# Kernel tuning notes

Measured on AMD Instinct MI355X. Metric: run time of the kernel, lower is better.

Reference implementation:

```python
import jax, jax.numpy as jnp
import numpy as np

B, C, H, W, CLASSES = 128, 30, 15, 15, 16
ROUTINGS = 3
IN_NUM_CAPS = 32 * 11 * 11  # 3872
IN_DIM, OUT_DIM = 8, 16


def squash(x, axis=-1):
    norm = jnp.linalg.norm(x, axis=axis, keepdims=True)
    scale = norm ** 2 / (1 + norm ** 2) / (norm + 1e-8)
    return scale * x


def conv2d(x, w, b):
    y = jax.lax.conv_general_dilated(x, w, (1, 1), 'VALID',
                                     dimension_numbers=('NCHW', 'OIHW', 'NCHW'))
    return y + b[None, :, None, None]


def setup_inputs() -> dict:
    key = jax.random.key(0)
    ks = jax.random.split(key, 12)
    x = jax.random.normal(ks[0], (B, C, H, W), jnp.float32)
    labels = jax.random.randint(ks[1], (B,), 0, CLASSES)
    y = jax.nn.one_hot(labels, CLASSES, dtype=jnp.float32)
    conv1_w = 0.05 * jax.random.normal(ks[2], (256, C, 3, 3), jnp.float32)
    conv1_b = jnp.zeros((256,), jnp.float32)
    bn_gamma = jnp.ones((256,), jnp.float32)
    bn_beta = jnp.zeros((256,), jnp.float32)
    conv2_w = 0.05 * jax.random.normal(ks[3], (256, 256, 3, 3), jnp.float32)
    conv2_b = jnp.zeros((256,), jnp.float32)
    caps_w = 0.01 * jax.random.normal(ks[4], (CLASSES, IN_NUM_CAPS, OUT_DIM, IN_DIM), jnp.float32)
    dec_w1 = 0.05 * jax.random.normal(ks[5], (OUT_DIM * CLASSES, 328), jnp.float32)
    dec_b1 = jnp.zeros((328,), jnp.float32)
    dec_w2 = 0.05 * jax.random.normal(ks[6], (328, 192), jnp.float32)
    dec_b2 = jnp.zeros((192,), jnp.float32)
    dec_w3 = 0.05 * jax.random.normal(ks[7], (192, C * H * W), jnp.float32)
    dec_b3 = jnp.zeros((C * H * W,), jnp.float32)
    return dict(x=x, y=y, conv1_w=conv1_w, conv1_b=conv1_b, bn_gamma=bn_gamma,
                bn_beta=bn_beta, conv2_w=conv2_w, conv2_b=conv2_b, caps_w=caps_w,
                dec_w1=dec_w1, dec_b1=dec_b1, dec_w2=dec_w2, dec_b2=dec_b2,
                dec_w3=dec_w3, dec_b3=dec_b3)


def reference(x, y, conv1_w, conv1_b, bn_gamma, bn_beta, conv2_w, conv2_b,
              caps_w, dec_w1, dec_b1, dec_w2, dec_b2, dec_w3, dec_b3):
    # conv stem: conv -> batchnorm (batch stats, train mode) -> relu
    h = conv2d(x, conv1_w, conv1_b)                        # [B,256,13,13]
    mean = h.mean(axis=(0, 2, 3), keepdims=True)
    var = h.var(axis=(0, 2, 3), keepdims=True)
    h = (h - mean) / jnp.sqrt(var + 1e-5)
    h = h * bn_gamma[None, :, None, None] + bn_beta[None, :, None, None]
    h = jax.nn.relu(h)

    # primary capsules
    p = conv2d(h, conv2_w, conv2_b)                        # [B,256,11,11]
    caps = squash(p.reshape(B, -1, IN_DIM))                # [B,3872,8]

    # dense capsule: prediction vectors + dynamic routing
    x_hat = jnp.einsum('onij,bnj->boni', caps_w, caps)     # [B,16,3872,16]
    x_hat_det = jax.lax.stop_gradient(x_hat)
    b_log = jnp.zeros(x_hat.shape[:3], x_hat.dtype)        # [B,16,3872]
    out = None
    for i in range(ROUTINGS):
        c = jax.nn.softmax(b_log, axis=1)
        xh = x_hat if i == ROUTINGS - 1 else x_hat_det
        out = squash(jnp.einsum('bon,bond->bod', c, xh))   # [B,16,16]
        if i < ROUTINGS - 1:
            b_log = b_log + jnp.einsum('bod,bond->bon', out, x_hat_det)

    length = jnp.linalg.norm(out, axis=-1)                 # [B,16]

    # decoder MLP on label-masked capsules
    masked = (out * y[:, :, None]).reshape(B, -1)          # [B,256]
    r = jax.nn.sigmoid(masked @ dec_w1 + dec_b1)
    r = jax.nn.sigmoid(r @ dec_w2 + dec_b2)
    recon = (r @ dec_w3 + dec_b3).reshape(B, C, H, W)
    return length, recon
```

## Files before the change

### kernel.cpp

```cpp
#include <hip/hip_runtime.h>
#include <hip/hip_bf16.h>

#define NB 128
#define CIN 30
#define HW 15
#define OC 256
#define H1 13
#define H2 11
#define NCAPS 3872
#define IND 8
#define OUTD 16
#define CLS 16
#define D1 328
#define D2 192
#define OUTPIX 6750
#define NSPLIT 121
#define NPB 32
#define RN 2
#define ROUNDS 16

typedef __attribute__((ext_vector_type(8))) short short8_t;
typedef __attribute__((ext_vector_type(4))) float f32x4;
typedef __attribute__((ext_vector_type(4))) unsigned int u32x4;

__device__ inline unsigned bf16rne(float f) {
  unsigned u = __builtin_bit_cast(unsigned, f);
  return (u + 0x7FFF + ((u >> 16) & 1)) >> 16;
}

#define BLO(u) __builtin_bit_cast(float, (unsigned)((u) << 16))
#define BHI(u) __builtin_bit_cast(float, (unsigned)((u) & 0xffff0000u))

__global__ __launch_bounds__(256) void pack_w1_k(const float* __restrict__ w,
    unsigned short* __restrict__ wpk1) {
  int tid = blockIdx.x * blockDim.x + threadIdx.x;
  int j = tid & 7;
  int oc = (tid >> 3) & 255;
  int kc = (tid >> 11) & 3;
  int tap = tid >> 13;
  int ic = kc * 8 + j;
  float v = (ic < CIN) ? w[((size_t)oc * CIN + ic) * 9 + tap] : 0.f;
  wpk1[tid] = (unsigned short)bf16rne(v);
}

__global__ __launch_bounds__(512, 1) void conv1_mfma_k(
    const float* __restrict__ x, const unsigned short* __restrict__ wpk1,
    const float* __restrict__ bias, float* __restrict__ h,
    float* __restrict__ hsum, float* __restrict__ hsum2) {
  __shared__ char smem[128 * 176 * 4];
  unsigned* hs32 = (unsigned*)smem;
  int bid = blockIdx.x;
  int b = bid >> 1;
  int nh = bid & 1;
  int t = threadIdx.x;
  int l = t & 63;
  int wid = t >> 6;

  if (t < 225) {
    const float* xb = x + (size_t)b * (CIN * 225);
#pragma unroll
    for (int icp = 0; icp < 15; icp++) {
      unsigned u0 = bf16rne(xb[(2 * icp) * 225 + t]);
      unsigned u1 = bf16rne(xb[(2 * icp + 1) * 225 + t]);
      hs32[t * 18 + icp] = u0 | (u1 << 16);
    }
    hs32[t * 18 + 15] = 0;
  }
  __syncthreads();

  int row = l & 15, kc = l >> 4;
  int ocb = nh * 128 + wid * 16;

  int arow[11];
#pragma unroll
  for (int mf = 0; mf < 11; mf++) {
    int m = mf * 16 + row;
    int pix = 0;
    if (m < 169) { int oy = m / 13, ox = m - oy * 13; pix = oy * HW + ox; }
    arow[mf] = pix * 72 + kc * 16;
  }

  f32x4 acc[11];
#pragma unroll
  for (int mf = 0; mf < 11; mf++) acc[mf] = (f32x4){0.f, 0.f, 0.f, 0.f};

  const size_t lanebase = ((size_t)ocb + row) * 8;
  const char* lds_base = (const char*)smem;

#pragma unroll
  for (int tap = 0; tap < 9; tap++) {
    const int ky = tap / 3, kx = tap % 3;
    const int koff = (ky * HW + kx) * 72;
    short8_t bfr = *(const short8_t*)(wpk1 + (size_t)(tap * 4 + kc) * 2048 + lanebase);
#pragma unroll
    for (int mf = 0; mf < 11; mf++) {
      short8_t af = *(const short8_t*)(lds_base + arow[mf] + koff);
      acc[mf] = __builtin_amdgcn_mfma_f32_16x16x32_bf16(af, bfr, acc[mf], 0, 0, 0);
    }
  }

  __syncthreads();
  float* cl = (float*)smem;
  {
    int ocl = wid * 16 + row;
#pragma unroll
    for (int mf = 0; mf < 11; mf++) {
      int m0 = mf * 16 + kc * 4;
      *(f32x4*)&cl[ocl * 176 + m0] = acc[mf];
    }
  }
  __syncthreads();
  for (int idx = t; idx < 128 * 169; idx += 512) {
    int ocl = idx / 169;
    int m = idx - ocl * 169;
    int oc = nh * 128 + ocl;
    h[((size_t)b * 256 + oc) * 169 + m] = cl[ocl * 176 + m] + bias[oc];
  }
  {
    int ocl = t >> 2, sub = t & 3;
    float bs = bias[nh * 128 + ocl];
    float s1 = 0.f, s2 = 0.f;
    int m0 = sub * 43, m1 = m0 + 43; if (m1 > 169) m1 = 169;
    for (int m = m0; m < m1; m++) {
      float v = cl[ocl * 176 + m] + bs;
      s1 += v; s2 += v * v;
    }
    s1 += __shfl_xor(s1, 1); s2 += __shfl_xor(s2, 1);
    s1 += __shfl_xor(s1, 2); s2 += __shfl_xor(s2, 2);
    if (sub == 0) {
      hsum[b * 256 + nh * 128 + ocl] = s1;
      hsum2[b * 256 + nh * 128 + ocl] = s2;
    }
  }
}

__global__ __launch_bounds__(128) void bn_finalize_k(const float* __restrict__ hsum,
    const float* __restrict__ hsum2, float* __restrict__ mean, float* __restrict__ istd) {
  int c = blockIdx.x * 128 + threadIdx.x;
  float s = 0.f, s2 = 0.f;
  for (int b = 0; b < NB; b++) {
    s += hsum[b * 256 + c];
    s2 += hsum2[b * 256 + c];
  }
  const float inv_n = 1.0f / (NB * H1 * H1);
  float m = s * inv_n;
  float v = s2 * inv_n - m * m;
  mean[c] = m;
  istd[c] = rsqrtf(v + 1e-5f);
}

__global__ __launch_bounds__(256) void pack_w2_k(const float* __restrict__ w,
    unsigned short* __restrict__ wpk) {
  int tid = blockIdx.x * blockDim.x + threadIdx.x;
  int e = tid & 7;
  int oc = (tid >> 3) & 255;
  int icchunk = (tid >> 11) & 31;
  int kykx = tid >> 16;
  int ic = icchunk * 8 + e;
  wpk[tid] = (unsigned short)bf16rne(w[((size_t)oc * 256 + ic) * 9 + kykx]);
}

__global__ __launch_bounds__(512, 1) void conv2_mfma_k(
    const float* __restrict__ h, const unsigned short* __restrict__ wpk,
    const float* __restrict__ bias, float* __restrict__ caps,
    const float* __restrict__ mean, const float* __restrict__ istd,
    const float* __restrict__ gamma, const float* __restrict__ beta) {
  __shared__ char smem[169 * 544];
  unsigned* hs32 = (unsigned*)smem;
  int bid = blockIdx.x;
  int b = bid >> 1;
  int nh = bid & 1;
  int t = threadIdx.x;
  int l = t & 63, wid = t >> 6;

  {
    const float* hb = h + (size_t)b * 256 * 169;
    for (int icp = wid; icp < 128; icp += 8) {
      const float* s0 = hb + (size_t)icp * 2 * 169;
      int c0i = icp * 2, c1i = icp * 2 + 1;
      float a0 = istd[c0i] * gamma[c0i], sh0 = beta[c0i] - mean[c0i] * a0;
      float a1 = istd[c1i] * gamma[c1i], sh1 = beta[c1i] - mean[c1i] * a1;
#pragma unroll
      for (int pb = 0; pb < 3; pb++) {
        int pix = pb * 64 + l;
        if (pix < 169) {
          float v0 = fmaxf(fmaf(s0[pix], a0, sh0), 0.f);
          float v1 = fmaxf(fmaf(s0[169 + pix], a1, sh1), 0.f);
          hs32[pix * 136 + icp] = bf16rne(v0) | (bf16rne(v1) << 16);
        }
      }
    }
  }
  __syncthreads();

  int wm = wid & 1;
  int wn = wid >> 1;
  int row = l & 15, kc = l >> 4;
  int ocb = nh * 128 + wn * 32;

  int abase[4];
#pragma unroll
  for (int mf = 0; mf < 4; mf++) {
    int m = wm * 64 + mf * 16 + row;
    int p0 = (m < 121) ? ((m / 11) * 13 + (m % 11)) : 0;
    abase[mf] = p0 * 544 + kc * 16;
  }

  f32x4 acc[4][2];
#pragma unroll
  for (int mf = 0; mf < 4; mf++)
#pragma unroll
    for (int nf = 0; nf < 2; nf++)
      acc[mf][nf] = (f32x4){0.f, 0.f, 0.f, 0.f};

  const size_t lanebase = ((size_t)kc * 256 + ocb + row) * 8;
  const char* lds_base = (const char*)smem;

  for (int ky = 0; ky < 3; ky++) {
    for (int kx = 0; kx < 3; kx++) {
      int r = ky * 3 + kx;
      int koff = (ky * 13 + kx) * 544;
#pragma unroll
      for (int ks = 0; ks < 8; ks++) {
        short8_t bfr[2];
#pragma unroll
        for (int nf = 0; nf < 2; nf++) {
          size_t idx = lanebase + (size_t)(r * 32 + ks * 4) * 2048 + nf * 128;
          bfr[nf] = *(const short8_t*)(wpk + idx);
        }
        short8_t af[4];
#pragma unroll
        for (int mf = 0; mf < 4; mf++)
          af[mf] = *(const short8_t*)(lds_base + (abase[mf] + koff + ks * 64));
#pragma unroll
        for (int mf = 0; mf < 4; mf++)
#pragma unroll
          for (int nf = 0; nf < 2; nf++)
            acc[mf][nf] = __builtin_amdgcn_mfma_f32_16x16x32_bf16(
                af[mf], bfr[nf], acc[mf][nf], 0, 0, 0);
      }
    }
  }

  __syncthreads();
  float* cl = (float*)smem;
#pragma unroll
  for (int nf = 0; nf < 2; nf++) {
    int ocl = wn * 32 + nf * 16 + row;
#pragma unroll
    for (int mf = 0; mf < 4; mf++) {
      int m0 = wm * 64 + mf * 16 + kc * 4;
      f32x4 v = acc[mf][nf];
      *(f32x4*)&cl[ocl * 132 + m0] = v;
    }
  }
  __syncthreads();
  for (int g = t; g < 1936; g += 512) {
    int base = g * 8;
    float v[8];
    float n2 = 0.f;
#pragma unroll
    for (int e = 0; e < 8; e++) {
      int idx = base + e;
      int q = idx / 121, rmd = idx - q * 121;
      float val = cl[q * 132 + rmd] + bias[nh * 128 + q];
      v[e] = val;
      n2 += val * val;
    }
    float nrm = sqrtf(n2);
    float scale = n2 / (1.f + n2) / (nrm + 1e-8f);
    float4 o0 = {v[0] * scale, v[1] * scale, v[2] * scale, v[3] * scale};
    float4 o1 = {v[4] * scale, v[5] * scale, v[6] * scale, v[7] * scale};
    float4* dst = (float4*)(caps + (((size_t)b * NCAPS) + nh * 1936 + g) * 8);
    dst[0] = o0; dst[1] = o1;
  }
}

__global__ __launch_bounds__(256) void pack_cw_k(const float* __restrict__ cw,
    unsigned short* __restrict__ Wp16) {
  int idx = blockIdx.x * blockDim.x + threadIdx.x;
  int i = idx & 15;
  int j = (idx >> 4) & 7;
  int o = (idx >> 7) & 15;
  int n = idx >> 11;
  Wp16[idx] = (unsigned short)bf16rne(cw[(((size_t)o * NCAPS + n) * 16 + i) * 8 + j]);
}

__global__ __launch_bounds__(256) void route_k(const float* __restrict__ caps,
    const unsigned short* __restrict__ Wp16, const float* __restrict__ osum,
    float* __restrict__ spart) {
  __shared__ unsigned short wl[2][RN * 2176];
  int id = blockIdx.x;
  int xcd = id & 7;
  int lin = (xcd < 4 ? xcd * 61 : 244 + (xcd - 4) * 60) + (id >> 3);
  int split = lin >> 2;
  int btile = lin & 3;
  int t = threadIdx.x;
  int o = t & 15;
  int bp = t >> 4;
  int b0 = btile * 32 + bp * 2;

  const float* opa = osum + (b0 * 16 + o) * 16;
  f32x4 oa0 = *(const f32x4*)(opa);
  f32x4 oa1 = *(const f32x4*)(opa + 4);
  f32x4 oa2 = *(const f32x4*)(opa + 8);
  f32x4 oa3 = *(const f32x4*)(opa + 12);
  const float* opb = opa + 256;
  f32x4 ob0 = *(const f32x4*)(opb);
  f32x4 ob1 = *(const f32x4*)(opb + 4);
  f32x4 ob2 = *(const f32x4*)(opb + 8);
  f32x4 ob3 = *(const f32x4*)(opb + 12);
  f32x4 sA0 = {0.f,0.f,0.f,0.f}, sA1 = {0.f,0.f,0.f,0.f};
  f32x4 sA2 = {0.f,0.f,0.f,0.f}, sA3 = {0.f,0.f,0.f,0.f};
  f32x4 sB0 = {0.f,0.f,0.f,0.f}, sB1 = {0.f,0.f,0.f,0.f};
  f32x4 sB2 = {0.f,0.f,0.f,0.f}, sB3 = {0.f,0.f,0.f,0.f};

  int nbeg = split * NPB;
  const u32x4* src = (const u32x4*)(Wp16 + (size_t)nbeg * 2048);

  int e0 = t, e1 = t + 256;
  int d0 = (e0 >> 8) * 2176 + ((e0 >> 4) & 15) * 136 + (e0 & 15) * 8;
  int d1 = (e1 >> 8) * 2176 + ((e1 >> 4) & 15) * 136 + (e1 & 15) * 8;

  {
    u32x4 v0 = src[e0], v1 = src[e1];
    *(u32x4*)&wl[0][d0] = v0;
    *(u32x4*)&wl[0][d1] = v1;
  }
  __syncthreads();

  for (int r = 0; r < ROUNDS; r++) {
    u32x4 nv0, nv1;
    if (r < ROUNDS - 1) {
      const u32x4* s2 = src + (r + 1) * 512;
      nv0 = s2[e0]; nv1 = s2[e1];
    }
    const unsigned short* wlb = wl[r & 1];
#pragma unroll
    for (int nl = 0; nl < RN; nl++) {
      int n = nbeg + r * RN + nl;
      const float4* cpa = (const float4*)(caps + ((size_t)b0 * NCAPS + n) * 8);
      const float4* cpb = (const float4*)(caps + ((size_t)(b0 + 1) * NCAPS + n) * 8);
      float4 cqa0 = cpa[0], cqa1 = cpa[1];
      float4 cqb0 = cpb[0], cqb1 = cpb[1];
      float caA[8] = {cqa0.x, cqa0.y, cqa0.z, cqa0.w, cqa1.x, cqa1.y, cqa1.z, cqa1.w};
      float caB[8] = {cqb0.x, cqb0.y, cqb0.z, cqb0.w, cqb1.x, cqb1.y, cqb1.z, cqb1.w};
      const unsigned short* wp = wlb + nl * 2176 + o * 136;
      f32x4 xa0 = {0.f,0.f,0.f,0.f}, xa1 = {0.f,0.f,0.f,0.f};
      f32x4 xa2 = {0.f,0.f,0.f,0.f}, xa3 = {0.f,0.f,0.f,0.f};
      f32x4 xb0 = {0.f,0.f,0.f,0.f}, xb1 = {0.f,0.f,0.f,0.f};
      f32x4 xb2 = {0.f,0.f,0.f,0.f}, xb3 = {0.f,0.f,0.f,0.f};
#pragma unroll
      for (int j = 0; j < 8; j++) {
        u32x4 wA = *(const u32x4*)(wp + j * 16);
        u32x4 wB = *(const u32x4*)(wp + j * 16 + 8);
        f32x4 w0 = {BLO(wA.x), BHI(wA.x), BLO(wA.y), BHI(wA.y)};
        f32x4 w1 = {BLO(wA.z), BHI(wA.z), BLO(wA.w), BHI(wA.w)};
        f32x4 w2 = {BLO(wB.x), BHI(wB.x), BLO(wB.y), BHI(wB.y)};
        f32x4 w3 = {BLO(wB.z), BHI(wB.z), BLO(wB.w), BHI(wB.w)};
        float cjA = caA[j], cjB = caB[j];
        xa0 += w0 * cjA; xa1 += w1 * cjA; xa2 += w2 * cjA; xa3 += w3 * cjA;
        xb0 += w0 * cjB; xb1 += w1 * cjB; xb2 += w2 * cjB; xb3 += w3 * cjB;
      }
      f32x4 pA = oa0 * xa0 + oa1 * xa1 + oa2 * xa2 + oa3 * xa3;
      f32x4 pB = ob0 * xb0 + ob1 * xb1 + ob2 * xb2 + ob3 * xb3;
      float blogA = (pA.x + pA.y) + (pA.z + pA.w);
      float blogB = (pB.x + pB.y) + (pB.z + pB.w);
      float eA = __expf(blogA);
      float eB = __expf(blogB);
      float ssA = eA, ssB = eB;
      ssA += __shfl_xor(ssA, 1); ssB += __shfl_xor(ssB, 1);
      ssA += __shfl_xor(ssA, 2); ssB += __shfl_xor(ssB, 2);
      ssA += __shfl_xor(ssA, 4); ssB += __shfl_xor(ssB, 4);
      ssA += __shfl_xor(ssA, 8); ssB += __shfl_xor(ssB, 8);
      float ccA = eA * __builtin_amdgcn_rcpf(ssA);
      float ccB = eB * __builtin_amdgcn_rcpf(ssB);
      sA0 += xa0 * ccA; sA1 += xa1 * ccA; sA2 += xa2 * ccA; sA3 += xa3 * ccA;
      sB0 += xb0 * ccB; sB1 += xb1 * ccB; sB2 += xb2 * ccB; sB3 += xb3 * ccB;
    }
    if (r < ROUNDS - 1) {
      unsigned short* dst = wl[(r + 1) & 1];
      *(u32x4*)&dst[d0] = nv0;
      *(u32x4*)&dst[d1] = nv1;
      __syncthreads();
    }
  }
  float* spA = spart + (((size_t)split * NB + b0) * 16 + o) * 16;
  *(f32x4*)spA = sA0; *(f32x4*)(spA + 4) = sA1;
  *(f32x4*)(spA + 8) = sA2; *(f32x4*)(spA + 12) = sA3;
  float* spB = spA + 256;
  *(f32x4*)spB = sB0; *(f32x4*)(spB + 4) = sB1;
  *(f32x4*)(spB + 8) = sB2; *(f32x4*)(spB + 12) = sB3;
}

__global__ __launch_bounds__(256) void combine_squash_k(const float* __restrict__ spart,
    float* __restrict__ osum, float* __restrict__ outbuf, const float* __restrict__ y,
    float* __restrict__ masked, float* __restrict__ length_out, int last) {
  int tid = blockIdx.x * blockDim.x + threadIdx.x;
  int i = tid & 15;
  int o = (tid >> 4) & 15;
  int b = tid >> 8;
  float s = 0.f;
  for (int k = 0; k < NSPLIT; k++) s += spart[(size_t)k * 32768 + tid];
  float n2 = s * s;
#pragma unroll
  for (int d = 1; d < 16; d <<= 1) n2 += __shfl_xor(n2, d);
  float nrm = sqrtf(n2);
  float scale = n2 / (1.f + n2) / (nrm + 1e-8f);
  float ov = scale * s;
  outbuf[tid] = ov;
  osum[tid] += ov;
  if (last) {
    masked[tid] = ov * y[b * 16 + o];
    if (i == 0) length_out[b * 16 + o] = scale * nrm;
  }
}

__global__ __launch_bounds__(256) void dec1_k(const float* __restrict__ masked,
    const float* __restrict__ w1, const float* __restrict__ b1, float* __restrict__ r1) {
  int tid = blockIdx.x * blockDim.x + threadIdx.x;
  if (tid >= NB * D1) return;
  int j = tid % D1;
  int b = tid / D1;
  const float* mp = masked + b * 256;
  float acc = b1[j];
  for (int k = 0; k < 256; k++) acc += mp[k] * w1[k * D1 + j];
  r1[tid] = 1.f / (1.f + __expf(-acc));
}

__global__ __launch_bounds__(256) void dec2_k(const float* __restrict__ r1,
    const float* __restrict__ w2, const float* __restrict__ b2, float* __restrict__ r2) {
  int tid = blockIdx.x * blockDim.x + threadIdx.x;
  if (tid >= NB * D2) return;
  int j = tid % D2;
  int b = tid / D2;
  const float* rp = r1 + b * D1;
  float acc = b2[j];
  for (int k = 0; k < D1; k++) acc += rp[k] * w2[k * D2 + j];
  r2[tid] = 1.f / (1.f + __expf(-acc));
}

__global__ __launch_bounds__(256) void dec3_k(const float* __restrict__ r2,
    const float* __restrict__ w3, const float* __restrict__ b3, float* __restrict__ recon) {
  __shared__ float r2s[D2 * 64];
  int mt = blockIdx.x, bh = blockIdx.y;
  int t = threadIdx.x;
  int b0 = bh * 64;
  for (int idx = t; idx < D2 * 64; idx += 256) {
    int bb = idx / D2, k = idx - bb * D2;
    r2s[k * 64 + bb] = r2[(b0 + bb) * D2 + k];
  }
  __syncthreads();
  int moff = t & 63, bg = t >> 6;
  int m = mt * 64 + moff;
  if (m >= OUTPIX) return;
  float acc[16];
#pragma unroll
  for (int q = 0; q < 16; q++) acc[q] = 0.f;
  for (int k = 0; k < D2; k++) {
    float wv = w3[k * OUTPIX + m];
    const float4* r4 = (const float4*)&r2s[k * 64 + bg * 16];
#pragma unroll
    for (int v = 0; v < 4; v++) {
      float4 rv = r4[v];
      acc[v * 4 + 0] += wv * rv.x;
      acc[v * 4 + 1] += wv * rv.y;
      acc[v * 4 + 2] += wv * rv.z;
      acc[v * 4 + 3] += wv * rv.w;
    }
  }
  float bias = b3[m];
#pragma unroll
  for (int q = 0; q < 16; q++) {
    int b = b0 + bg * 16 + q;
    recon[(size_t)b * OUTPIX + m] = acc[q] + bias;
  }
}

extern "C" void kernel_launch(void* const* d_in, const int* in_sizes, int n_in,
                              void* d_out, int out_size, void* d_ws, size_t ws_size,
                              hipStream_t stream) {
  const float* x      = (const float*)d_in[0];
  const float* y      = (const float*)d_in[1];
  const float* conv1w = (const float*)d_in[2];
  const float* conv1b = (const float*)d_in[3];
  const float* gamma  = (const float*)d_in[4];
  const float* beta   = (const float*)d_in[5];
  const float* conv2w = (const float*)d_in[6];
  const float* conv2b = (const float*)d_in[7];
  const float* capsw  = (const float*)d_in[8];
  const float* w1     = (const float*)d_in[9];
  const float* b1     = (const float*)d_in[10];
  const float* w2     = (const float*)d_in[11];
  const float* b2     = (const float*)d_in[12];
  const float* w3     = (const float*)d_in[13];
  const float* b3     = (const float*)d_in[14];

  float* ws = (float*)d_ws;
  float* h      = ws;
  float* p      = h + 5537792;
  float* caps   = p + 3964928;
  float* mean   = caps + 3964928;
  float* istd   = mean + 256;
  float* osum   = istd + 256;
  float* spart  = osum + 32768;
  float* outb   = spart + 3964928;
  float* masked = outb + 32768;
  float* r1     = masked + 32768;
  float* r2     = r1 + 41984;
  unsigned short* wpk = (unsigned short*)(r2 + 24576);
  unsigned short* wpk1 = wpk + 589824;
  unsigned short* Wp16 = (unsigned short*)ws;
  float* hsum  = spart;
  float* hsum2 = spart + 32768;

  float* length_out = (float*)d_out;
  float* recon      = (float*)d_out + 2048;

  pack_w1_k<<<73728 / 256, 256, 0, stream>>>(conv1w, wpk1);
  conv1_mfma_k<<<256, 512, 0, stream>>>(x, wpk1, conv1b, h, hsum, hsum2);
  bn_finalize_k<<<2, 128, 0, stream>>>(hsum, hsum2, mean, istd);

  pack_w2_k<<<589824 / 256, 256, 0, stream>>>(conv2w, wpk);
  conv2_mfma_k<<<256, 512, 0, stream>>>(h, wpk, conv2b, caps, mean, istd, gamma, beta);

  pack_cw_k<<<7929856 / 256, 256, 0, stream>>>(capsw, Wp16);

  hipMemsetAsync(osum, 0, 32768 * sizeof(float), stream);
  for (int it = 0; it < 3; ++it) {
    route_k<<<484, 256, 0, stream>>>(caps, Wp16, osum, spart);
    combine_squash_k<<<128, 256, 0, stream>>>(spart, osum, outb, y, masked,
                                              length_out, it == 2 ? 1 : 0);
  }

  dec1_k<<<(NB * D1 + 255) / 256, 256, 0, stream>>>(masked, w1, b1, r1);
  dec2_k<<<(NB * D2 + 255) / 256, 256, 0, stream>>>(r1, w2, b2, r2);
  dec3_k<<<dim3((OUTPIX + 63) / 64, 2), 256, 0, stream>>>(r2, w3, b3, recon);
}
```

Baseline: 363.7 us.

## Merge weight-pack kernels, halve conv1 LDS, widen routing rounds, unroll combine

Fuses the conv1 and conv2 weight-packing kernels into one launch. Halves conv1's shared-memory staging by writing results out in two 64-channel passes, and drops the one-block-per-CU launch bound so more blocks can be resident. Makes the routing kernel stage four capsules per round instead of two, halving the number of barriered rounds. Splits the cross-split reduction in combine_squash across four independent accumulators. Costs are an extra barrier pair in conv1, more registers and LDS in the routing kernel, and a slightly different summation order.

```diff
diff --git a/kernel.cpp b/kernel.cpp
--- a/kernel.cpp
+++ b/kernel.cpp
@@ -16,8 +16,8 @@
 #define OUTPIX 6750
 #define NSPLIT 121
 #define NPB 32
-#define RN 2
-#define ROUNDS 16
+#define RN 4
+#define ROUNDS 8
 
 typedef __attribute__((ext_vector_type(8))) short short8_t;
 typedef __attribute__((ext_vector_type(4))) float f32x4;
@@ -31,23 +31,34 @@
 #define BLO(u) __builtin_bit_cast(float, (unsigned)((u) << 16))
 #define BHI(u) __builtin_bit_cast(float, (unsigned)((u) & 0xffff0000u))
 
-__global__ __launch_bounds__(256) void pack_w1_k(const float* __restrict__ w,
-    unsigned short* __restrict__ wpk1) {
+__global__ __launch_bounds__(256) void pack_w12_k(const float* __restrict__ w1,
+    const float* __restrict__ w2, unsigned short* __restrict__ wpk1,
+    unsigned short* __restrict__ wpk) {
   int tid = blockIdx.x * blockDim.x + threadIdx.x;
-  int j = tid & 7;
-  int oc = (tid >> 3) & 255;
-  int kc = (tid >> 11) & 3;
-  int tap = tid >> 13;
-  int ic = kc * 8 + j;
-  float v = (ic < CIN) ? w[((size_t)oc * CIN + ic) * 9 + tap] : 0.f;
-  wpk1[tid] = (unsigned short)bf16rne(v);
-}
-
-__global__ __launch_bounds__(512, 1) void conv1_mfma_k(
+  if (tid < 73728) {
+    int j = tid & 7;
+    int oc = (tid >> 3) & 255;
+    int kc = (tid >> 11) & 3;
+    int tap = tid >> 13;
+    int ic = kc * 8 + j;
+    float v = (ic < CIN) ? w1[((size_t)oc * CIN + ic) * 9 + tap] : 0.f;
+    wpk1[tid] = (unsigned short)bf16rne(v);
+  } else {
+    int t2 = tid - 73728;
+    int e = t2 & 7;
+    int oc = (t2 >> 3) & 255;
+    int icchunk = (t2 >> 11) & 31;
+    int kykx = t2 >> 16;
+    int ic = icchunk * 8 + e;
+    wpk[t2] = (unsigned short)bf16rne(w2[((size_t)oc * 256 + ic) * 9 + kykx]);
+  }
+}
+
+__global__ __launch_bounds__(512) void conv1_mfma_k(
     const float* __restrict__ x, const unsigned short* __restrict__ wpk1,
     const float* __restrict__ bias, float* __restrict__ h,
     float* __restrict__ hsum, float* __restrict__ hsum2) {
-  __shared__ char smem[128 * 176 * 4];
+  __shared__ char smem[64 * 176 * 4];
   unsigned* hs32 = (unsigned*)smem;
   int bid = blockIdx.x;
   int b = bid >> 1;
@@ -69,7 +80,6 @@
   __syncthreads();
 
   int row = l & 15, kc = l >> 4;
-  int ocb = nh * 128 + wid * 16;
 
   int arow[11];
 #pragma unroll
@@ -84,7 +94,7 @@
 #pragma unroll
   for (int mf = 0; mf < 11; mf++) acc[mf] = (f32x4){0.f, 0.f, 0.f, 0.f};
 
-  const size_t lanebase = ((size_t)ocb + row) * 8;
+  const size_t lanebase = ((size_t)(nh * 128 + wid * 16) + row) * 8;
   const char* lds_base = (const char*)smem;
 
 #pragma unroll
@@ -99,37 +109,41 @@
     }
   }
 
-  __syncthreads();
   float* cl = (float*)smem;
-  {
-    int ocl = wid * 16 + row;
-#pragma unroll
-    for (int mf = 0; mf < 11; mf++) {
-      int m0 = mf * 16 + kc * 4;
-      *(f32x4*)&cl[ocl * 176 + m0] = acc[mf];
-    }
-  }
-  __syncthreads();
-  for (int idx = t; idx < 128 * 169; idx += 512) {
-    int ocl = idx / 169;
-    int m = idx - ocl * 169;
-    int oc = nh * 128 + ocl;
-    h[((size_t)b * 256 + oc) * 169 + m] = cl[ocl * 176 + m] + bias[oc];
-  }
-  {
-    int ocl = t >> 2, sub = t & 3;
-    float bs = bias[nh * 128 + ocl];
-    float s1 = 0.f, s2 = 0.f;
-    int m0 = sub * 43, m1 = m0 + 43; if (m1 > 169) m1 = 169;
-    for (int m = m0; m < m1; m++) {
-      float v = cl[ocl * 176 + m] + bs;
-      s1 += v; s2 += v * v;
-    }
-    s1 += __shfl_xor(s1, 1); s2 += __shfl_xor(s2, 1);
-    s1 += __shfl_xor(s1, 2); s2 += __shfl_xor(s2, 2);
-    if (sub == 0) {
-      hsum[b * 256 + nh * 128 + ocl] = s1;
-      hsum2[b * 256 + nh * 128 + ocl] = s2;
+  for (int half = 0; half < 2; half++) {
+    __syncthreads();
+    if ((wid >> 2) == half) {
+      int ocl = (wid & 3) * 16 + row;
+#pragma unroll
+      for (int mf = 0; mf < 11; mf++) {
+        int m0 = mf * 16 + kc * 4;
+        *(f32x4*)&cl[ocl * 176 + m0] = acc[mf];
+      }
+    }
+    __syncthreads();
+    for (int idx = t; idx < 64 * 169; idx += 512) {
+      int ocl = idx / 169;
+      int m = idx - ocl * 169;
+      int oc = nh * 128 + half * 64 + ocl;
+      h[((size_t)b * 256 + oc) * 169 + m] = cl[ocl * 176 + m] + bias[oc];
+    }
+    {
+      int ocl = t >> 3, sub = t & 7;
+      int oc = nh * 128 + half * 64 + ocl;
+      float bs = bias[oc];
+      float s1 = 0.f, s2 = 0.f;
+      int m0 = sub * 22, m1 = m0 + 22; if (m1 > 169) m1 = 169;
+      for (int m = m0; m < m1; m++) {
+        float v = cl[ocl * 176 + m] + bs;
+        s1 += v; s2 += v * v;
+      }
+      s1 += __shfl_xor(s1, 1); s2 += __shfl_xor(s2, 1);
+      s1 += __shfl_xor(s1, 2); s2 += __shfl_xor(s2, 2);
+      s1 += __shfl_xor(s1, 4); s2 += __shfl_xor(s2, 4);
+      if (sub == 0) {
+        hsum[b * 256 + oc] = s1;
+        hsum2[b * 256 + oc] = s2;
+      }
     }
   }
 }
@@ -147,17 +161,6 @@
   float v = s2 * inv_n - m * m;
   mean[c] = m;
   istd[c] = rsqrtf(v + 1e-5f);
-}
-
-__global__ __launch_bounds__(256) void pack_w2_k(const float* __restrict__ w,
-    unsigned short* __restrict__ wpk) {
-  int tid = blockIdx.x * blockDim.x + threadIdx.x;
-  int e = tid & 7;
-  int oc = (tid >> 3) & 255;
-  int icchunk = (tid >> 11) & 31;
-  int kykx = tid >> 16;
-  int ic = icchunk * 8 + e;
-  wpk[tid] = (unsigned short)bf16rne(w[((size_t)oc * 256 + ic) * 9 + kykx]);
 }
 
 __global__ __launch_bounds__(512, 1) void conv2_mfma_k(
@@ -318,22 +321,24 @@
   int nbeg = split * NPB;
   const u32x4* src = (const u32x4*)(Wp16 + (size_t)nbeg * 2048);
 
-  int e0 = t, e1 = t + 256;
+  int e0 = t, e1 = t + 256, e2 = t + 512, e3 = t + 768;
   int d0 = (e0 >> 8) * 2176 + ((e0 >> 4) & 15) * 136 + (e0 & 15) * 8;
   int d1 = (e1 >> 8) * 2176 + ((e1 >> 4) & 15) * 136 + (e1 & 15) * 8;
+  int d2 = (e2 >> 8) * 2176 + ((e2 >> 4) & 15) * 136 + (e2 & 15) * 8;
+  int d3 = (e3 >> 8) * 2176 + ((e3 >> 4) & 15) * 136 + (e3 & 15) * 8;
 
   {
-    u32x4 v0 = src[e0], v1 = src[e1];
-    *(u32x4*)&wl[0][d0] = v0;
-    *(u32x4*)&wl[0][d1] = v1;
+    u32x4 v0 = src[e0], v1 = src[e1], v2 = src[e2], v3 = src[e3];
+    *(u32x4*)&wl[0][d0] = v0; *(u32x4*)&wl[0][d1] = v1;
+    *(u32x4*)&wl[0][d2] = v2; *(u32x4*)&wl[0][d3] = v3;
   }
   __syncthreads();
 
   for (int r = 0; r < ROUNDS; r++) {
-    u32x4 nv0, nv1;
+    u32x4 nv0, nv1, nv2, nv3;
     if (r < ROUNDS - 1) {
-      const u32x4* s2 = src + (r + 1) * 512;
-      nv0 = s2[e0]; nv1 = s2[e1];
+      const u32x4* s2 = src + (r + 1) * 1024;
+      nv0 = s2[e0]; nv1 = s2[e1]; nv2 = s2[e2]; nv3 = s2[e3];
     }
     const unsigned short* wlb = wl[r & 1];
 #pragma unroll
@@ -380,8 +385,8 @@
     }
     if (r < ROUNDS - 1) {
       unsigned short* dst = wl[(r + 1) & 1];
-      *(u32x4*)&dst[d0] = nv0;
-      *(u32x4*)&dst[d1] = nv1;
+      *(u32x4*)&dst[d0] = nv0; *(u32x4*)&dst[d1] = nv1;
+      *(u32x4*)&dst[d2] = nv2; *(u32x4*)&dst[d3] = nv3;
       __syncthreads();
     }
   }
@@ -400,8 +405,16 @@
   int i = tid & 15;
   int o = (tid >> 4) & 15;
   int b = tid >> 8;
-  float s = 0.f;
-  for (int k = 0; k < NSPLIT; k++) s += spart[(size_t)k * 32768 + tid];
+  float a0 = 0.f, a1 = 0.f, a2 = 0.f, a3 = 0.f;
+  int k = 0;
+  for (; k + 4 <= NSPLIT; k += 4) {
+    a0 += spart[(size_t)k * 32768 + tid];
+    a1 += spart[(size_t)(k + 1) * 32768 + tid];
+    a2 += spart[(size_t)(k + 2) * 32768 + tid];
+    a3 += spart[(size_t)(k + 3) * 32768 + tid];
+  }
+  float s = (a0 + a1) + (a2 + a3);
+  for (; k < NSPLIT; k++) s += spart[(size_t)k * 32768 + tid];
   float n2 = s * s;
 #pragma unroll
   for (int d = 1; d < 16; d <<= 1) n2 += __shfl_xor(n2, d);
@@ -517,11 +530,9 @@
   float* length_out = (float*)d_out;
   float* recon      = (float*)d_out + 2048;
 
-  pack_w1_k<<<73728 / 256, 256, 0, stream>>>(conv1w, wpk1);
+  pack_w12_k<<<(73728 + 589824) / 256, 256, 0, stream>>>(conv1w, conv2w, wpk1, wpk);
   conv1_mfma_k<<<256, 512, 0, stream>>>(x, wpk1, conv1b, h, hsum, hsum2);
   bn_finalize_k<<<2, 128, 0, stream>>>(hsum, hsum2, mean, istd);
-
-  pack_w2_k<<<589824 / 256, 256, 0, stream>>>(conv2w, wpk);
   conv2_mfma_k<<<256, 512, 0, stream>>>(h, wpk, conv2b, caps, mean, istd, gamma, beta);
 
   pack_cw_k<<<7929856 / 256, 256, 0, stream>>>(capsw, Wp16);
```

Measured after the change: 412.9 us. 13.5% more time.
